# Performance work log

Hardware: AMD Instinct MI355X
Metric: run time of the kernel (lower is better)

The kernel has to match this reference:

```python
import jax, jax.numpy as jnp
import numpy as np

B, N, S, C1, C2 = 8, 8192, 2048, 128, 256
IN_CH = C1 + C2
MLP = [256, 128]
EPS_INTERP = 1e-8
EPS_BN = 1e-5


def setup_inputs() -> dict:
    key = jax.random.key(0)
    ks = jax.random.split(key, 8)
    inp = {
        "xyz1": jax.random.normal(ks[0], (B, 3, N), dtype=jnp.float32),
        "xyz2": jax.random.normal(ks[1], (B, 3, S), dtype=jnp.float32),
        "points1": jax.random.normal(ks[2], (B, C1, N), dtype=jnp.float32),
        "points2": jax.random.normal(ks[3], (B, C2, S), dtype=jnp.float32),
        # Conv1d(k=1) weights as [out, in] matrices, plus BN gamma/beta
        "W1": jax.random.normal(ks[4], (MLP[0], IN_CH), dtype=jnp.float32) * 0.02,
        "b1": jnp.zeros((MLP[0],), dtype=jnp.float32),
        "g1": jnp.ones((MLP[0],), dtype=jnp.float32),
        "be1": jnp.zeros((MLP[0],), dtype=jnp.float32),
        "W2": jax.random.normal(ks[5], (MLP[1], MLP[0]), dtype=jnp.float32) * 0.02,
        "b2": jnp.zeros((MLP[1],), dtype=jnp.float32),
        "g2": jnp.ones((MLP[1],), dtype=jnp.float32),
        "be2": jnp.zeros((MLP[1],), dtype=jnp.float32),
    }
    return inp


def _conv_bn_relu(x, W, b, g, be):
    # x: [B, N, Cin]; 1x1 Conv1d == per-point matmul; BN over (batch, length) per channel (training-mode stats)
    y = jnp.einsum('bnc,oc->bno', x, W) + b
    m = jnp.mean(y, axis=(0, 1))
    v = jnp.var(y, axis=(0, 1))
    return jax.nn.relu((y - m) * jax.lax.rsqrt(v + EPS_BN) * g + be)


def reference(xyz1, xyz2, points1, points2, W1, b1, g1, be1, W2, b2, g2, be2):
    x1 = xyz1.transpose(0, 2, 1)   # [B, N, 3]
    x2 = xyz2.transpose(0, 2, 1)   # [B, S, 3]
    p2 = points2.transpose(0, 2, 1)  # [B, S, C2]
    p1 = points1.transpose(0, 2, 1)  # [B, N, C1]

    # squared pairwise distances [B, N, S]
    d = (jnp.sum(x1 * x1, axis=-1, keepdims=True)
         - 2.0 * jnp.einsum('bnd,bsd->bns', x1, x2)
         + jnp.sum(x2 * x2, axis=-1)[:, None, :])

    # 3 nearest neighbors (smallest distances)
    neg_d, idx = jax.lax.top_k(-d, 3)          # idx: [B, N, 3]
    d3 = -neg_d                                 # [B, N, 3]
    recip = 1.0 / (d3 + EPS_INTERP)
    w = recip / jnp.sum(recip, axis=-1, keepdims=True)  # [B, N, 3]

    gathered = jax.vmap(lambda p, i: p[i])(p2, idx)     # [B, N, 3, C2]
    interp = jnp.sum(gathered * w[..., None], axis=2)   # [B, N, C2]

    x = jnp.concatenate([p1, interp], axis=-1)          # [B, N, C1+C2]
    x = _conv_bn_relu(x, W1, b1, g1, be1)
    x = _conv_bn_relu(x, W2, b2, g2, be2)
    return x.transpose(0, 2, 1)                         # [B, mlp[-1], N]
```

## Files before the change

### kernel.cpp

```cpp
#include <hip/hip_runtime.h>
#include <stdint.h>

#define B_ 8
#define N_ 8192
#define S_ 2048
#define C1_ 128
#define C2_ 256
#define IN_ 384
#define H1_ 256
#define H2_ 128
#define M_ (B_*N_)

typedef short bf16x8 __attribute__((ext_vector_type(8)));
typedef float f32x4 __attribute__((ext_vector_type(4)));

__device__ __forceinline__ float bf2f(unsigned short s){
  union { unsigned int u; float f; } x; x.u = ((unsigned int)s) << 16; return x.f;
}
__device__ __forceinline__ unsigned short f2bf(float f){
  union { float f; unsigned int u; } x; x.f = f;
  unsigned int u = x.u;
  unsigned int r = (u + 0x7FFFu + ((u >> 16) & 1u)) >> 16;
  return (unsigned short)r;
}

__device__ __forceinline__ size_t fragaddr(int m, int k, int K){
  return ((size_t)((m >> 4) * (K >> 5) + (k >> 5)) << 9)
       + (size_t)((((k >> 3) & 3) << 7) + ((m & 15) << 3) + (k & 7));
}

__device__ __forceinline__ void gload_lds16(const unsigned short* g, unsigned short* l){
  __builtin_amdgcn_global_load_lds(
      (const __attribute__((address_space(1))) unsigned int*)g,
      (__attribute__((address_space(3))) unsigned int*)l, 16, 0, 0);
}

__global__ __launch_bounds__(256) void prep_fused_kernel(const float* W1, const float* W2,
                                                         const float* p2, const float* p1,
                                                         const float* xyz2, float4* ptsg,
                                                         unsigned short* w1b, unsigned short* w2b,
                                                         float* stats, unsigned short* p2t,
                                                         unsigned short* x){
  __shared__ float tile[32][33];
  int bx = blockIdx.x;
  if (bx < 384){
    int i = bx * 256 + threadIdx.x;
    if (i < 256*384){
      int row = i / 384, col = i - row*384;
      w1b[fragaddr(row, col, 384)] = f2bf(W1[i]);
    }
    if (i < 128*256){
      int row = i >> 8, col = i & 255;
      w2b[fragaddr(row, col, 256)] = f2bf(W2[i]);
    }
    if (i < 1536) stats[i] = 0.f;
    return;
  }
  if (bx < 448){
    int i = (bx - 384) * 256 + threadIdx.x;
    int b = i >> 11, s = i & 2047;
    const float* src = xyz2 + (size_t)b * 3 * S_;
    float px = src[s], py = src[S_ + s], pz = src[2*S_ + s];
    ptsg[i] = make_float4(-2.f*px, -2.f*py, -2.f*pz, px*px + py*py + pz*pz);
    return;
  }
  int tx = threadIdx.x & 31, ty = threadIdx.x >> 5;
  if (bx < 4544){
    int id = bx - 448;
    int b = id >> 9, rem = id & 511;
    int l0 = (rem & 63) * 32, r0 = (rem >> 6) * 32;
    const float* src = p2 + (size_t)b * C2_ * S_;
    #pragma unroll
    for (int rr = ty; rr < 32; rr += 8)
      tile[rr][tx] = src[(size_t)(r0 + rr) * S_ + l0 + tx];
    __syncthreads();
    unsigned short* dst = p2t + (size_t)b * S_ * C2_;
    #pragma unroll
    for (int rr = ty; rr < 32; rr += 8)
      dst[(size_t)(l0 + rr) * C2_ + r0 + tx] = f2bf(tile[tx][rr]);
    return;
  }
  {
    int id = bx - 4544;
    int b = id >> 10, rem = id & 1023;
    int l0 = (rem & 255) * 32, r0 = (rem >> 8) * 32;
    const float* src = p1 + (size_t)b * C1_ * N_;
    #pragma unroll
    for (int rr = ty; rr < 32; rr += 8)
      tile[rr][tx] = src[(size_t)(r0 + rr) * N_ + l0 + tx];
    __syncthreads();
    #pragma unroll
    for (int rr = ty; rr < 32; rr += 8){
      int g = b * N_ + l0 + rr;
      size_t a = ((size_t)((g >> 4)*12 + (r0 >> 5)) << 9)
               + (size_t)((((tx >> 3) & 3) << 7) + ((g & 15) << 3) + (tx & 7));
      x[a] = f2bf(tile[tx][rr]);
    }
  }
}

#define PIECES_ 8
#define SPP_ (S_ / PIECES_)

__device__ __forceinline__ void insert_k(float& k0, float& k1, float& k2, float x){
  k2 = __builtin_amdgcn_fmed3f(k1, k2, x);
  k1 = __builtin_amdgcn_fmed3f(k0, k1, x);
  k0 = fminf(k0, x);
}

__device__ __forceinline__ void insert3(float& d0, float& d1, float& d2,
                                        int& i0, int& i1, int& i2,
                                        float x, int s){
  bool b0 = x < d0, b1 = x < d1, b2 = x < d2;
  i2 = b1 ? i1 : (b2 ? s : i2);
  i1 = b0 ? i0 : (b1 ? s : i1);
  i0 = b0 ? s : i0;
  d2 = __builtin_amdgcn_fmed3f(d1, d2, x);
  d1 = __builtin_amdgcn_fmed3f(d0, d1, x);
  d0 = fminf(d0, x);
}

__global__ __launch_bounds__(256, 8) void knn_kernel(const float* __restrict__ xyz1,
                                                     const float4* __restrict__ ptsg,
                                                     float* __restrict__ partd,
                                                     int* __restrict__ parti){
  __shared__ float4 pts[SPP_];
  int b = blockIdx.y, piece = blockIdx.z;
  int n = blockIdx.x * 256 + threadIdx.x;
  int base = piece * SPP_;
  const float4* __restrict__ cp = ptsg + (size_t)b * S_ + base;
  pts[threadIdx.x] = cp[threadIdx.x];

  const float* __restrict__ x1 = xyz1 + (size_t)b * 3 * N_;
  float ax = x1[n], ay = x1[N_ + n], az = x1[2*N_ + n];
  float x1sq = ax*ax + ay*ay + az*az;

  const float KINIT = __uint_as_float(0x7F000000u);
  float k[2][3];
  k[0][0]=k[0][1]=k[0][2]=KINIT;
  k[1][0]=k[1][1]=k[1][2]=KINIT;

  for (int s = 0; s < SPP_; s += 8){
    #pragma unroll
    for (int u = 0; u < 8; u++){
      float4 c = cp[s + u];
      float dd = fmaf(ax, c.x, fmaf(ay, c.y, fmaf(az, c.z, c.w + x1sq)));
      float key = __uint_as_float((__float_as_uint(dd) & 0xFFFFFF00u) | (unsigned)(s + u));
      int L = u & 1;
      insert_k(k[L][0], k[L][1], k[L][2], key);
    }
  }
  float e0 = k[0][0], e1 = k[0][1], e2 = k[0][2];
  insert_k(e0, e1, e2, k[1][0]);
  insert_k(e0, e1, e2, k[1][1]);
  insert_k(e0, e1, e2, k[1][2]);

  __syncthreads();
  float ed[3]; int ei[3];
  float ev[3] = {e0, e1, e2};
  #pragma unroll
  for (int j = 0; j < 3; j++){
    int li = (int)(__float_as_uint(ev[j]) & 0xFFu);
    float4 c = pts[li];
    float dd = fmaf(ax, c.x, fmaf(ay, c.y, fmaf(az, c.z, c.w + x1sq)));
    ed[j] = fmaxf(dd, 0.f);
    ei[j] = base + li;
  }

  size_t g = (size_t)b * N_ + n;
  partd[(piece*3 + 0)*(size_t)M_ + g] = ed[0];
  partd[(piece*3 + 1)*(size_t)M_ + g] = ed[1];
  partd[(piece*3 + 2)*(size_t)M_ + g] = ed[2];
  parti[(piece*3 + 0)*(size_t)M_ + g] = ei[0];
  parti[(piece*3 + 1)*(size_t)M_ + g] = ei[1];
  parti[(piece*3 + 2)*(size_t)M_ + g] = ei[2];
}

__global__ __launch_bounds__(256) void interp_kernel(const float* partd, const int* parti,
                                                     const unsigned short* p2t, unsigned short* x){
  __shared__ int   sidx[16][3];
  __shared__ float swgt[16][3];
  int t = threadIdx.x;
  int base = blockIdx.x * 16;
  if (t < 16){
    size_t g = (size_t)base + t;
    float d0 = partd[0*(size_t)M_ + g], d1 = partd[1*(size_t)M_ + g], d2 = partd[2*(size_t)M_ + g];
    int   i0 = parti[0*(size_t)M_ + g], i1 = parti[1*(size_t)M_ + g], i2 = parti[2*(size_t)M_ + g];
    #pragma unroll
    for (int p = 1; p < PIECES_; p++)
      #pragma unroll
      for (int j = 0; j < 3; j++)
        insert3(d0, d1, d2, i0, i1, i2,
                partd[(p*3 + j)*(size_t)M_ + g], parti[(p*3 + j)*(size_t)M_ + g]);
    float r0 = 1.f/(d0 + 1e-8f), r1 = 1.f/(d1 + 1e-8f), r2 = 1.f/(d2 + 1e-8f);
    float rs = 1.f/(r0 + r1 + r2);
    sidx[t][0] = i0; sidx[t][1] = i1; sidx[t][2] = i2;
    swgt[t][0] = r0*rs; swgt[t][1] = r1*rs; swgt[t][2] = r2*rs;
  }
  __syncthreads();
  size_t suboff = (size_t)((((t >> 3) & 3) << 7) + (t & 7));
  for (int k = 0; k < 16; k++){
    int g = base + k;
    int b = g >> 13;
    const unsigned short* p = p2t + (size_t)b * S_ * C2_;
    float v = swgt[k][0]*bf2f(p[(size_t)sidx[k][0]*C2_ + t])
            + swgt[k][1]*bf2f(p[(size_t)sidx[k][1]*C2_ + t])
            + swgt[k][2]*bf2f(p[(size_t)sidx[k][2]*C2_ + t]);
    size_t a = ((size_t)((g >> 4)*12 + 4 + (t >> 5)) << 9) + suboff + (size_t)((g & 15) << 3);
    x[a] = f2bf(v);
  }
}

__device__ __forceinline__ bf16x8 bn_relu_frag(bf16x8 v, const float* a, const float* c, int kb){
  union { bf16x8 h; unsigned short s[8]; } u; u.h = v;
  union { float4 v4; float f[4]; } a0, a1, c0, c1;
  a0.v4 = *(const float4*)(a + kb);  a1.v4 = *(const float4*)(a + kb + 4);
  c0.v4 = *(const float4*)(c + kb);  c1.v4 = *(const float4*)(c + kb + 4);
  #pragma unroll
  for (int j = 0; j < 4; j++){
    float f0 = fmaf(a0.f[j], bf2f(u.s[j]),     c0.f[j]);
    float f1 = fmaf(a1.f[j], bf2f(u.s[j + 4]), c1.f[j]);
    u.s[j]     = f2bf(fmaxf(f0, 0.f));
    u.s[j + 4] = f2bf(fmaxf(f1, 0.f));
  }
  return u.h;
}

template<int K, bool HAS_AFF, bool OUT_FRAG>
__global__ __launch_bounds__(256) void gemm_lds_kernel(
    const unsigned short* __restrict__ A, const unsigned short* __restrict__ Wf,
    unsigned short* __restrict__ Cout, int Ntot,
    float* pbuf, const float* aff_a, const float* aff_c)
{
  constexpr int KT = K / 32;
  __shared__ unsigned short smA[128*64];
  __shared__ unsigned short smB[128*64];
  __shared__ float ldsStat[256];

  const int t = threadIdx.x;
  const int lane = t & 63, wave = t >> 6;
  const int ln = lane & 15, lq = lane >> 4;
  const int wm = wave >> 1, wn = wave & 1;
  const int mtb = blockIdx.x * 8;
  const int ntb = blockIdx.y * 8;
  const int mtw = mtb + wm * 4;
  const int n0  = blockIdx.y * 128 + wn * 64;

  ldsStat[t] = 0.f;

  const int c0 = 2*wave, c1 = 2*wave + 1;

  const f32x4 fzero = {0.f, 0.f, 0.f, 0.f};
  f32x4 acc[4][4];
  #pragma unroll
  for (int i = 0; i < 4; i++)
    #pragma unroll
    for (int j = 0; j < 4; j++) acc[i][j] = fzero;

  for (int kk = 0; kk < KT; kk += 2){
    #pragma unroll
    for (int q = 0; q < 2; q++){
      gload_lds16(A  + (((size_t)((mtb + c0)*KT + kk + q)) << 9) + lane*8,
                  &smA[((c0*2 + q) << 9) + lane*8]);
      gload_lds16(A  + (((size_t)((mtb + c1)*KT + kk + q)) << 9) + lane*8,
                  &smA[((c1*2 + q) << 9) + lane*8]);
      gload_lds16(Wf + (((size_t)((ntb + c0)*KT + kk + q)) << 9) + lane*8,
                  &smB[((c0*2 + q) << 9) + lane*8]);
      gload_lds16(Wf + (((size_t)((ntb + c1)*KT + kk + q)) << 9) + lane*8,
                  &smB[((c1*2 + q) << 9) + lane*8]);
    }
    __syncthreads();
    #pragma unroll
    for (int q = 0; q < 2; q++){
      bf16x8 af[4], bfr[4];
      #pragma unroll
      for (int i = 0; i < 4; i++)
        af[i] = *(const bf16x8*)(&smA[(((wm*4 + i)*2 + q) << 9) + lane*8]);
      #pragma unroll
      for (int j = 0; j < 4; j++)
        bfr[j] = *(const bf16x8*)(&smB[(((wn*4 + j)*2 + q) << 9) + lane*8]);
      if (HAS_AFF){
        const int kb = (kk + q)*32 + lq*8;
        #pragma unroll
        for (int i = 0; i < 4; i++) af[i] = bn_relu_frag(af[i], aff_a, aff_c, kb);
      }
      #pragma unroll
      for (int i = 0; i < 4; i++)
        #pragma unroll
        for (int j = 0; j < 4; j++)
          acc[i][j] = __builtin_amdgcn_mfma_f32_16x16x32_bf16(af[i], bfr[j], acc[i][j], 0, 0, 0);
    }
    __syncthreads();
  }

  #pragma unroll
  for (int j = 0; j < 4; j++){
    int ncol = n0 + j*16 + ln;
    float s = 0.f, q = 0.f;
    #pragma unroll
    for (int i = 0; i < 4; i++){
      #pragma unroll
      for (int r = 0; r < 4; r++){
        float v = acc[i][j][r];
        if (OUT_FRAG){
          size_t a = ((size_t)((mtw + i)*8 + (ncol >> 5)) << 9)
                   + (size_t)((((ncol >> 3) & 3) << 7) + ((lq*4 + r) << 3) + (ncol & 7));
          Cout[a] = f2bf(v);
        } else {
          Cout[((size_t)((mtw + i)*16 + lq*4 + r)) * Ntot + ncol] = f2bf(v);
        }
        s += v; q += v*v;
      }
    }
    s += __shfl_xor(s, 16); s += __shfl_xor(s, 32);
    q += __shfl_xor(q, 16); q += __shfl_xor(q, 32);
    if (lq == 0){
      int colLocal = wn*64 + j*16 + ln;
      atomicAdd(&ldsStat[colLocal], s);
      atomicAdd(&ldsStat[128 + colLocal], q);
    }
  }
  __syncthreads();
  pbuf[((size_t)(blockIdx.y * gridDim.x + blockIdx.x) << 8) + t] = ldsStat[t];
}

__global__ __launch_bounds__(256) void finalize_kernel(const float* pbuf, const float* g,
                                                       const float* be, float* a_out,
                                                       float* c_out){
  __shared__ float red[8];
  int c = blockIdx.x, t = threadIdx.x;
  int grp = c >> 7, lc = c & 127;
  const float* base = pbuf + ((size_t)(grp * 512) << 8);
  float s = base[((size_t)t << 8) + lc]       + base[((size_t)(t + 256) << 8) + lc];
  float q = base[((size_t)t << 8) + 128 + lc] + base[((size_t)(t + 256) << 8) + 128 + lc];
  #pragma unroll
  for (int o = 1; o < 64; o <<= 1){ s += __shfl_xor(s, o); q += __shfl_xor(q, o); }
  int w = t >> 6;
  if ((t & 63) == 0){ red[w] = s; red[4 + w] = q; }
  __syncthreads();
  if (t == 0){
    s = red[0] + red[1] + red[2] + red[3];
    q = red[4] + red[5] + red[6] + red[7];
    float mean = s * (1.f / M_);
    float var  = q * (1.f / M_) - mean*mean;
    float a = g[c] * rsqrtf(var + 1e-5f);
    a_out[c] = a;
    c_out[c] = fmaf(-mean, a, be[c]);
  }
}

__global__ __launch_bounds__(256) void out_kernel(const unsigned short* y2, const float* a2,
                                                  const float* c2, float* out){
  __shared__ float lds[64][65];
  int t  = threadIdx.x;
  int b  = blockIdx.z;
  int n0 = blockIdx.y * 64;
  int c0 = blockIdx.x * 64;
  int cc = t & 63, tr = t >> 6;
  float a = a2[c0 + cc], cadd = c2[c0 + cc];
  #pragma unroll
  for (int ph = 0; ph < 16; ph++){
    int nr = tr + ph*4;
    unsigned short v = y2[((size_t)(b*N_ + n0 + nr)) * H2_ + c0 + cc];
    lds[nr][cc] = fmaxf(fmaf(a, bf2f(v), cadd), 0.f);
  }
  __syncthreads();
  #pragma unroll
  for (int ph = 0; ph < 16; ph++){
    int cr = tr + ph*4;
    out[((size_t)(b*H2_ + c0 + cr)) * N_ + n0 + cc] = lds[cc][cr];
  }
}

extern "C" void kernel_launch(void* const* d_in, const int* in_sizes, int n_in,
                              void* d_out, int out_size, void* d_ws, size_t ws_size,
                              hipStream_t stream){
  const float* xyz1 = (const float*)d_in[0];
  const float* xyz2 = (const float*)d_in[1];
  const float* p1   = (const float*)d_in[2];
  const float* p2   = (const float*)d_in[3];
  const float* W1   = (const float*)d_in[4];
  const float* g1   = (const float*)d_in[6];
  const float* be1  = (const float*)d_in[7];
  const float* W2   = (const float*)d_in[8];
  const float* g2   = (const float*)d_in[10];
  const float* be2  = (const float*)d_in[11];
  float* out = (float*)d_out;

  char* ws = (char*)d_ws;
  unsigned short* x    = (unsigned short*)(ws + 0);
  unsigned short* p2t  = (unsigned short*)(ws + 50331648);
  unsigned short* y1   = (unsigned short*)(ws + 58720256);
  unsigned short* y2   = (unsigned short*)(ws + 92274688);
  unsigned short* w1b  = (unsigned short*)(ws + 109051904);
  unsigned short* w2b  = (unsigned short*)(ws + 109248512);
  float*          stats= (float*)(ws + 110886912);
  float* a1   = stats + 768;  float* c1  = stats + 1024;
  float* a2   = stats + 1280; float* c2  = stats + 1408;
  float* partd = (float*)y1;
  int*   parti = (int*)(y1 + 6291456);
  float4* ptsg = (float4*)y2;
  float* pbuf1 = (float*)p2t;
  float* pbuf2 = (float*)x;

  prep_fused_kernel<<<12736, 256, 0, stream>>>(W1, W2, p2, p1, xyz2, ptsg, w1b, w2b, stats, p2t, x);
  knn_kernel<<<dim3(32, 8, PIECES_), 256, 0, stream>>>(xyz1, ptsg, partd, parti);
  interp_kernel<<<4096, 256, 0, stream>>>(partd, parti, p2t, x);
  gemm_lds_kernel<384, false, true><<<dim3(512, 2), 256, 0, stream>>>(
      x, w1b, y1, 256, pbuf1, nullptr, nullptr);
  finalize_kernel<<<256, 256, 0, stream>>>(pbuf1, g1, be1, a1, c1);
  gemm_lds_kernel<256, true, false><<<dim3(512, 1), 256, 0, stream>>>(
      y1, w2b, y2, 128, pbuf2, a1, c1);
  finalize_kernel<<<128, 256, 0, stream>>>(pbuf2, g2, be2, a2, c2);
  out_kernel<<<dim3(2, 128, 8), 256, 0, stream>>>(y2, a2, c2, out);
}
```

Baseline: 250.3 us.

## Fuse prep and kNN kernels into one interleaved launch with LDS point reads

Merges the weight/feature conversion kernel and the kNN partial top-3 kernel into a single launch. Blocks are interleaved as 16 kNN blocks per 99 prep blocks, so compute-bound kNN work overlaps with bandwidth-bound transposes. Each kNN block now computes its own point table into LDS, and the inner loop reads candidates from LDS instead of global memory. This removes one launch and the ptsg round trip, but kNN blocks lose the occupancy hint of 8 blocks per CU and share a 4KB LDS union with the transpose tiles.

```diff
diff --git a/kernel.cpp b/kernel.cpp
--- a/kernel.cpp
+++ b/kernel.cpp
@@ -33,70 +33,6 @@
   __builtin_amdgcn_global_load_lds(
       (const __attribute__((address_space(1))) unsigned int*)g,
       (__attribute__((address_space(3))) unsigned int*)l, 16, 0, 0);
-}
-
-__global__ __launch_bounds__(256) void prep_fused_kernel(const float* W1, const float* W2,
-                                                         const float* p2, const float* p1,
-                                                         const float* xyz2, float4* ptsg,
-                                                         unsigned short* w1b, unsigned short* w2b,
-                                                         float* stats, unsigned short* p2t,
-                                                         unsigned short* x){
-  __shared__ float tile[32][33];
-  int bx = blockIdx.x;
-  if (bx < 384){
-    int i = bx * 256 + threadIdx.x;
-    if (i < 256*384){
-      int row = i / 384, col = i - row*384;
-      w1b[fragaddr(row, col, 384)] = f2bf(W1[i]);
-    }
-    if (i < 128*256){
-      int row = i >> 8, col = i & 255;
-      w2b[fragaddr(row, col, 256)] = f2bf(W2[i]);
-    }
-    if (i < 1536) stats[i] = 0.f;
-    return;
-  }
-  if (bx < 448){
-    int i = (bx - 384) * 256 + threadIdx.x;
-    int b = i >> 11, s = i & 2047;
-    const float* src = xyz2 + (size_t)b * 3 * S_;
-    float px = src[s], py = src[S_ + s], pz = src[2*S_ + s];
-    ptsg[i] = make_float4(-2.f*px, -2.f*py, -2.f*pz, px*px + py*py + pz*pz);
-    return;
-  }
-  int tx = threadIdx.x & 31, ty = threadIdx.x >> 5;
-  if (bx < 4544){
-    int id = bx - 448;
-    int b = id >> 9, rem = id & 511;
-    int l0 = (rem & 63) * 32, r0 = (rem >> 6) * 32;
-    const float* src = p2 + (size_t)b * C2_ * S_;
-    #pragma unroll
-    for (int rr = ty; rr < 32; rr += 8)
-      tile[rr][tx] = src[(size_t)(r0 + rr) * S_ + l0 + tx];
-    __syncthreads();
-    unsigned short* dst = p2t + (size_t)b * S_ * C2_;
-    #pragma unroll
-    for (int rr = ty; rr < 32; rr += 8)
-      dst[(size_t)(l0 + rr) * C2_ + r0 + tx] = f2bf(tile[tx][rr]);
-    return;
-  }
-  {
-    int id = bx - 4544;
-    int b = id >> 10, rem = id & 1023;
-    int l0 = (rem & 255) * 32, r0 = (rem >> 8) * 32;
-    const float* src = p1 + (size_t)b * C1_ * N_;
-    #pragma unroll
-    for (int rr = ty; rr < 32; rr += 8)
-      tile[rr][tx] = src[(size_t)(r0 + rr) * N_ + l0 + tx];
-    __syncthreads();
-    #pragma unroll
-    for (int rr = ty; rr < 32; rr += 8){
-      int g = b * N_ + l0 + rr;
-      size_t a = ((size_t)((g >> 4)*12 + (r0 >> 5)) << 9)
-               + (size_t)((((tx >> 3) & 3) << 7) + ((g & 15) << 3) + (tx & 7));
-      x[a] = f2bf(tile[tx][rr]);
-    }
-  }
 }
 
 #define PIECES_ 8
@@ -120,60 +56,124 @@
   d0 = fminf(d0, x);
 }
 
-__global__ __launch_bounds__(256, 8) void knn_kernel(const float* __restrict__ xyz1,
-                                                     const float4* __restrict__ ptsg,
-                                                     float* __restrict__ partd,
-                                                     int* __restrict__ parti){
-  __shared__ float4 pts[SPP_];
-  int b = blockIdx.y, piece = blockIdx.z;
-  int n = blockIdx.x * 256 + threadIdx.x;
-  int base = piece * SPP_;
-  const float4* __restrict__ cp = ptsg + (size_t)b * S_ + base;
-  pts[threadIdx.x] = cp[threadIdx.x];
-
-  const float* __restrict__ x1 = xyz1 + (size_t)b * 3 * N_;
-  float ax = x1[n], ay = x1[N_ + n], az = x1[2*N_ + n];
-  float x1sq = ax*ax + ay*ay + az*az;
-
-  const float KINIT = __uint_as_float(0x7F000000u);
-  float k[2][3];
-  k[0][0]=k[0][1]=k[0][2]=KINIT;
-  k[1][0]=k[1][1]=k[1][2]=KINIT;
-
-  for (int s = 0; s < SPP_; s += 8){
-    #pragma unroll
-    for (int u = 0; u < 8; u++){
-      float4 c = cp[s + u];
+__global__ __launch_bounds__(256) void prep_knn_fused(
+    const float* W1, const float* W2, const float* p2, const float* p1,
+    const float* xyz1, const float* xyz2,
+    unsigned short* w1b, unsigned short* w2b, float* stats,
+    unsigned short* p2t, unsigned short* x,
+    float* partd, int* parti)
+{
+  __shared__ __align__(16) char smraw[4224];
+  float (*tile)[33] = reinterpret_cast<float(*)[33]>(smraw);
+  float4* pts = reinterpret_cast<float4*>(smraw);
+
+  const int per = blockIdx.x / 115;
+  const int r   = blockIdx.x % 115;
+  const int t   = threadIdx.x;
+
+  if (r < 16){
+    int kid = per*16 + r;
+    int nb = kid & 31, b = (kid >> 5) & 7, piece = kid >> 8;
+    int n = nb*256 + t;
+    int base = piece * SPP_;
+    const float* x2 = xyz2 + (size_t)b * 3 * S_;
+    {
+      float px = x2[base + t], py = x2[S_ + base + t], pz = x2[2*S_ + base + t];
+      pts[t] = make_float4(-2.f*px, -2.f*py, -2.f*pz, px*px + py*py + pz*pz);
+    }
+    __syncthreads();
+    const float* x1 = xyz1 + (size_t)b * 3 * N_;
+    float ax = x1[n], ay = x1[N_ + n], az = x1[2*N_ + n];
+    float x1sq = ax*ax + ay*ay + az*az;
+
+    const float KINIT = __uint_as_float(0x7F000000u);
+    float k[2][3];
+    k[0][0]=k[0][1]=k[0][2]=KINIT;
+    k[1][0]=k[1][1]=k[1][2]=KINIT;
+
+    for (int s = 0; s < SPP_; s += 8){
+      #pragma unroll
+      for (int u = 0; u < 8; u++){
+        float4 c = pts[s + u];
+        float dd = fmaf(ax, c.x, fmaf(ay, c.y, fmaf(az, c.z, c.w + x1sq)));
+        float key = __uint_as_float((__float_as_uint(dd) & 0xFFFFFF00u) | (unsigned)(s + u));
+        int L = u & 1;
+        insert_k(k[L][0], k[L][1], k[L][2], key);
+      }
+    }
+    float e0 = k[0][0], e1 = k[0][1], e2 = k[0][2];
+    insert_k(e0, e1, e2, k[1][0]);
+    insert_k(e0, e1, e2, k[1][1]);
+    insert_k(e0, e1, e2, k[1][2]);
+
+    float ed[3]; int ei[3];
+    float ev[3] = {e0, e1, e2};
+    #pragma unroll
+    for (int j = 0; j < 3; j++){
+      int li = (int)(__float_as_uint(ev[j]) & 0xFFu);
+      float4 c = pts[li];
       float dd = fmaf(ax, c.x, fmaf(ay, c.y, fmaf(az, c.z, c.w + x1sq)));
-      float key = __uint_as_float((__float_as_uint(dd) & 0xFFFFFF00u) | (unsigned)(s + u));
-      int L = u & 1;
-      insert_k(k[L][0], k[L][1], k[L][2], key);
-    }
-  }
-  float e0 = k[0][0], e1 = k[0][1], e2 = k[0][2];
-  insert_k(e0, e1, e2, k[1][0]);
-  insert_k(e0, e1, e2, k[1][1]);
-  insert_k(e0, e1, e2, k[1][2]);
-
-  __syncthreads();
-  float ed[3]; int ei[3];
-  float ev[3] = {e0, e1, e2};
-  #pragma unroll
-  for (int j = 0; j < 3; j++){
-    int li = (int)(__float_as_uint(ev[j]) & 0xFFu);
-    float4 c = pts[li];
-    float dd = fmaf(ax, c.x, fmaf(ay, c.y, fmaf(az, c.z, c.w + x1sq)));
-    ed[j] = fmaxf(dd, 0.f);
-    ei[j] = base + li;
-  }
-
-  size_t g = (size_t)b * N_ + n;
-  partd[(piece*3 + 0)*(size_t)M_ + g] = ed[0];
-  partd[(piece*3 + 1)*(size_t)M_ + g] = ed[1];
-  partd[(piece*3 + 2)*(size_t)M_ + g] = ed[2];
-  parti[(piece*3 + 0)*(size_t)M_ + g] = ei[0];
-  parti[(piece*3 + 1)*(size_t)M_ + g] = ei[1];
-  parti[(piece*3 + 2)*(size_t)M_ + g] = ei[2];
+      ed[j] = fmaxf(dd, 0.f);
+      ei[j] = base + li;
+    }
+
+    size_t g = (size_t)b * N_ + n;
+    partd[(piece*3 + 0)*(size_t)M_ + g] = ed[0];
+    partd[(piece*3 + 1)*(size_t)M_ + g] = ed[1];
+    partd[(piece*3 + 2)*(size_t)M_ + g] = ed[2];
+    parti[(piece*3 + 0)*(size_t)M_ + g] = ei[0];
+    parti[(piece*3 + 1)*(size_t)M_ + g] = ei[1];
+    parti[(piece*3 + 2)*(size_t)M_ + g] = ei[2];
+    return;
+  }
+
+  const int pid = per*99 + (r - 16);
+  if (pid < 384){
+    int i = pid * 256 + t;
+    if (i < 256*384){
+      int row = i / 384, col = i - row*384;
+      w1b[fragaddr(row, col, 384)] = f2bf(W1[i]);
+    }
+    if (i < 128*256){
+      int row = i >> 8, col = i & 255;
+      w2b[fragaddr(row, col, 256)] = f2bf(W2[i]);
+    }
+    if (i < 1536) stats[i] = 0.f;
+    return;
+  }
+  int tx = t & 31, ty = t >> 5;
+  if (pid < 4480){
+    int id = pid - 384;
+    int b = id >> 9, rem = id & 511;
+    int l0 = (rem & 63) * 32, r0 = (rem >> 6) * 32;
+    const float* src = p2 + (size_t)b * C2_ * S_;
+    #pragma unroll
+    for (int rr = ty; rr < 32; rr += 8)
+      tile[rr][tx] = src[(size_t)(r0 + rr) * S_ + l0 + tx];
+    __syncthreads();
+    unsigned short* dst = p2t + (size_t)b * S_ * C2_;
+    #pragma unroll
+    for (int rr = ty; rr < 32; rr += 8)
+      dst[(size_t)(l0 + rr) * C2_ + r0 + tx] = f2bf(tile[tx][rr]);
+    return;
+  }
+  {
+    int id = pid - 4480;
+    int b = id >> 10, rem = id & 1023;
+    int l0 = (rem & 255) * 32, r0 = (rem >> 8) * 32;
+    const float* src = p1 + (size_t)b * C1_ * N_;
+    #pragma unroll
+    for (int rr = ty; rr < 32; rr += 8)
+      tile[rr][tx] = src[(size_t)(r0 + rr) * N_ + l0 + tx];
+    __syncthreads();
+    #pragma unroll
+    for (int rr = ty; rr < 32; rr += 8){
+      int g = b * N_ + l0 + rr;
+      size_t a = ((size_t)((g >> 4)*12 + (r0 >> 5)) << 9)
+               + (size_t)((((tx >> 3) & 3) << 7) + ((g & 15) << 3) + (tx & 7));
+      x[a] = f2bf(tile[tx][rr]);
+    }
+  }
 }
 
 __global__ __launch_bounds__(256) void interp_kernel(const float* partd, const int* parti,
@@ -399,12 +399,11 @@
   float* a2   = stats + 1280; float* c2  = stats + 1408;
   float* partd = (float*)y1;
   int*   parti = (int*)(y1 + 6291456);
-  float4* ptsg = (float4*)y2;
   float* pbuf1 = (float*)p2t;
   float* pbuf2 = (float*)x;
 
-  prep_fused_kernel<<<12736, 256, 0, stream>>>(W1, W2, p2, p1, xyz2, ptsg, w1b, w2b, stats, p2t, x);
-  knn_kernel<<<dim3(32, 8, PIECES_), 256, 0, stream>>>(xyz1, ptsg, partd, parti);
+  prep_knn_fused<<<14720, 256, 0, stream>>>(W1, W2, p2, p1, xyz1, xyz2,
+                                            w1b, w2b, stats, p2t, x, partd, parti);
   interp_kernel<<<4096, 256, 0, stream>>>(partd, parti, p2t, x);
   gemm_lds_kernel<384, false, true><<<dim3(512, 2), 256, 0, stream>>>(
       x, w1b, y1, 256, pbuf1, nullptr, nullptr);
```

Result: faster. 242.3 us (-3.2%).
